# Performance work log

Hardware: AMD Instinct MI355X
Metric: run time of the kernel (lower is better)

## Reference

```python
import jax, jax.numpy as jnp
import numpy as np

MARGIN = 0.3
N_CLASSES = 256
N_SAMPLES = 32
D = 2048

def setup_inputs() -> dict:
    key = jax.random.key(0)
    k1, k2 = jax.random.split(key)
    embeddings = jax.random.normal(k1, (2 * N_CLASSES * N_SAMPLES, D), dtype=jnp.float32)
    target = jax.random.randint(k2, (2 * N_CLASSES * N_SAMPLES,), 0, N_CLASSES, dtype=jnp.int64 if jax.config.jax_enable_x64 else jnp.int32)
    return {"embeddings": embeddings, "target": target, "margin": MARGIN, "n_classes": N_CLASSES, "n_samples": N_SAMPLES}

def reference(embeddings, target, margin, n_classes, n_samples):
    # target is unused by the original forward (kept for signature fidelity).
    d = embeddings.shape[-1]
    # [C, 2, S, D]: slot 0 = positives, slot 1 = negatives per class
    e = embeddings.reshape(n_classes, 2, n_samples, d)
    pos, neg = e[:, 0], e[:, 1]                      # [C, S, D]
    anchor = pos.mean(axis=1, keepdims=True)          # [C, 1, D]
    ap = jnp.sqrt(jnp.sum((pos - anchor) ** 2, axis=-1))           # [C, S]
    neg_d2 = jnp.sum((neg - anchor) ** 2, axis=-1)                 # [C, S]
    # hardest negative: min squared distance to anchor -> its sqrt is an_distance
    an = jnp.sqrt(jnp.min(neg_d2, axis=1, keepdims=True))          # [C, 1]
    losses = jnp.sum(jax.nn.relu(ap - an + margin) ** 2, axis=1)   # [C]
    return losses.mean()
```

## Files before the change

kernel.cpp:

```cpp
#include <hip/hip_runtime.h>

#define NCLS 256
#define NSMP 32
#define DIM  2048
#define DV   (DIM / 4)
#define BLK  512
#define ROWS 520
#define PF   8

__global__ __launch_bounds__(BLK, 2)
void ccl_kernel(const float* __restrict__ emb,
                const float* __restrict__ margin_p,
                float* __restrict__ out) {
    const int c   = blockIdx.x;
    const int tid = threadIdx.x;

    __shared__ float part[NSMP * ROWS];
    __shared__ float d2p[NSMP];
    __shared__ float d2n[NSMP];

    const float4* pos = (const float4*)(emb + (size_t)c * 2 * NSMP * DIM);
    const float4* neg = pos + (size_t)NSMP * DV;

    float4 x[NSMP];
    #pragma unroll
    for (int i = 0; i < NSMP; ++i) x[i] = pos[(size_t)i * DV + tid];

    float4 a = make_float4(0.f, 0.f, 0.f, 0.f);
    #pragma unroll
    for (int i = 0; i < NSMP; ++i) {
        a.x += x[i].x; a.y += x[i].y; a.z += x[i].z; a.w += x[i].w;
    }
    const float inv = 1.0f / (float)NSMP;
    a.x *= inv; a.y *= inv; a.z *= inv; a.w *= inv;

    float4 nb[PF];
    #pragma unroll
    for (int j = 0; j < PF; ++j) nb[j] = neg[(size_t)j * DV + tid];

    #pragma unroll
    for (int i = 0; i < NSMP; ++i) {
        float dx = x[i].x - a.x, dy = x[i].y - a.y;
        float dz = x[i].z - a.z, dw = x[i].w - a.w;
        part[i * ROWS + tid] = dx * dx + dy * dy + dz * dz + dw * dw;
    }
    __syncthreads();

    const int s   = tid >> 4;
    const int c16 = tid & 15;
    {
        float sum = 0.f;
        #pragma unroll
        for (int k = 0; k < 8; ++k) {
            float4 v = *(const float4*)&part[s * ROWS + c16 * 4 + k * 64];
            sum += v.x + v.y + v.z + v.w;
        }
        #pragma unroll
        for (int off = 8; off >= 1; off >>= 1) sum += __shfl_xor(sum, off, 64);
        if (c16 == 0) d2p[s] = sum;
    }
    __syncthreads();

    #pragma unroll
    for (int i = 0; i < NSMP; ++i) {
        float4 n = nb[i & (PF - 1)];
        if (i + PF < NSMP) nb[i & (PF - 1)] = neg[(size_t)(i + PF) * DV + tid];
        float dx = n.x - a.x, dy = n.y - a.y;
        float dz = n.z - a.z, dw = n.w - a.w;
        part[i * ROWS + tid] = dx * dx + dy * dy + dz * dz + dw * dw;
    }
    __syncthreads();

    {
        float sum = 0.f;
        #pragma unroll
        for (int k = 0; k < 8; ++k) {
            float4 v = *(const float4*)&part[s * ROWS + c16 * 4 + k * 64];
            sum += v.x + v.y + v.z + v.w;
        }
        #pragma unroll
        for (int off = 8; off >= 1; off >>= 1) sum += __shfl_xor(sum, off, 64);
        if (c16 == 0) d2n[s] = sum;
    }
    __syncthreads();

    if (tid < 64) {
        float nd = (tid < NSMP) ? d2n[tid] : 3.4e38f;
        #pragma unroll
        for (int off = 32; off >= 1; off >>= 1) nd = fminf(nd, __shfl_xor(nd, off, 64));
        const float an = sqrtf(nd);
        const float margin = margin_p[0];

        float l = 0.f;
        if (tid < NSMP) {
            float ap = sqrtf(d2p[tid]);
            float v  = fmaxf(ap - an + margin, 0.f);
            l = v * v;
        }
        #pragma unroll
        for (int off = 32; off >= 1; off >>= 1) l += __shfl_xor(l, off, 64);
        if (tid == 0) atomicAdd(out, l * (1.0f / (float)NCLS));
    }
}

extern "C" void kernel_launch(void* const* d_in, const int* in_sizes, int n_in,
                              void* d_out, int out_size, void* d_ws, size_t ws_size,
                              hipStream_t stream) {
    const float* emb    = (const float*)d_in[0];
    const float* margin = (const float*)d_in[2];
    float* out = (float*)d_out;

    hipMemsetAsync(out, 0, sizeof(float), stream);
    ccl_kernel<<<NCLS, BLK, 0, stream>>>(emb, margin, out);
}
```

Measured before the change: 198.0 us.

## Split feature dimension across two blocks per class with a separate finalize kernel

Each class is now handled by two 256-thread blocks, each covering half of the feature dimension. Per-sample partial squared distances are combined with atomics into a workspace buffer. A second single-block kernel then computes the hardest negative, the hinge loss and the mean. This halves per-block shared memory and gives finer scheduling granularity, but adds a workspace memset, atomics and an extra kernel launch.

```diff
diff --git a/kernel.cpp b/kernel.cpp
--- a/kernel.cpp
+++ b/kernel.cpp
@@ -1,26 +1,28 @@
 #include <hip/hip_runtime.h>
 
-#define NCLS 256
-#define NSMP 32
-#define DIM  2048
-#define DV   (DIM / 4)
-#define BLK  512
-#define ROWS 520
-#define PF   8
+#define NCLS  256
+#define NSMP  32
+#define DIM   2048
+#define DV    (DIM / 4)
+#define SPLIT 2
+#define CHUNK (DV / SPLIT)
+#define BLK   256
+#define ROWS  264
+#define PF    8
 
 __global__ __launch_bounds__(BLK, 2)
-void ccl_kernel(const float* __restrict__ emb,
-                const float* __restrict__ margin_p,
-                float* __restrict__ out) {
+void ccl_partial(const float* __restrict__ emb,
+                 float* __restrict__ ws_pos,
+                 float* __restrict__ ws_neg) {
     const int c   = blockIdx.x;
+    const int h   = blockIdx.y;
     const int tid = threadIdx.x;
 
     __shared__ float part[NSMP * ROWS];
-    __shared__ float d2p[NSMP];
-    __shared__ float d2n[NSMP];
 
-    const float4* pos = (const float4*)(emb + (size_t)c * 2 * NSMP * DIM);
-    const float4* neg = pos + (size_t)NSMP * DV;
+    const float* base = emb + (size_t)c * 2 * NSMP * DIM + (size_t)h * (CHUNK * 4);
+    const float4* pos = (const float4*)base;
+    const float4* neg = (const float4*)(base + (size_t)NSMP * DIM);
 
     float4 x[NSMP];
     #pragma unroll
@@ -46,18 +48,18 @@
     }
     __syncthreads();
 
-    const int s   = tid >> 4;
-    const int c16 = tid & 15;
+    const int s  = tid >> 3;
+    const int c8 = tid & 7;
     {
         float sum = 0.f;
         #pragma unroll
         for (int k = 0; k < 8; ++k) {
-            float4 v = *(const float4*)&part[s * ROWS + c16 * 4 + k * 64];
+            float4 v = *(const float4*)&part[s * ROWS + c8 * 4 + k * 32];
             sum += v.x + v.y + v.z + v.w;
         }
         #pragma unroll
-        for (int off = 8; off >= 1; off >>= 1) sum += __shfl_xor(sum, off, 64);
-        if (c16 == 0) d2p[s] = sum;
+        for (int off = 4; off >= 1; off >>= 1) sum += __shfl_xor(sum, off, 64);
+        if (c8 == 0) atomicAdd(&ws_pos[c * NSMP + s], sum);
     }
     __syncthreads();
 
@@ -75,31 +77,49 @@
         float sum = 0.f;
         #pragma unroll
         for (int k = 0; k < 8; ++k) {
-            float4 v = *(const float4*)&part[s * ROWS + c16 * 4 + k * 64];
+            float4 v = *(const float4*)&part[s * ROWS + c8 * 4 + k * 32];
             sum += v.x + v.y + v.z + v.w;
         }
         #pragma unroll
-        for (int off = 8; off >= 1; off >>= 1) sum += __shfl_xor(sum, off, 64);
-        if (c16 == 0) d2n[s] = sum;
+        for (int off = 4; off >= 1; off >>= 1) sum += __shfl_xor(sum, off, 64);
+        if (c8 == 0) atomicAdd(&ws_neg[c * NSMP + s], sum);
     }
+}
+
+__global__ __launch_bounds__(NCLS)
+void ccl_final(const float* __restrict__ ws_pos,
+               const float* __restrict__ ws_neg,
+               const float* __restrict__ margin_p,
+               float* __restrict__ out) {
+    const int c    = threadIdx.x;
+    const int wave = c >> 6;
+    const int lane = c & 63;
+    __shared__ float red[NCLS / 64];
+
+    const float margin = margin_p[0];
+
+    float nd = 3.4e38f;
+    #pragma unroll
+    for (int i = 0; i < NSMP; ++i) nd = fminf(nd, ws_neg[c * NSMP + i]);
+    const float an = sqrtf(nd);
+
+    float l = 0.f;
+    #pragma unroll
+    for (int i = 0; i < NSMP; ++i) {
+        float ap = sqrtf(ws_pos[c * NSMP + i]);
+        float v  = fmaxf(ap - an + margin, 0.f);
+        l += v * v;
+    }
+
+    #pragma unroll
+    for (int off = 32; off >= 1; off >>= 1) l += __shfl_xor(l, off, 64);
+    if (lane == 0) red[wave] = l;
     __syncthreads();
-
-    if (tid < 64) {
-        float nd = (tid < NSMP) ? d2n[tid] : 3.4e38f;
+    if (c == 0) {
+        float t = 0.f;
         #pragma unroll
-        for (int off = 32; off >= 1; off >>= 1) nd = fminf(nd, __shfl_xor(nd, off, 64));
-        const float an = sqrtf(nd);
-        const float margin = margin_p[0];
-
-        float l = 0.f;
-        if (tid < NSMP) {
-            float ap = sqrtf(d2p[tid]);
-            float v  = fmaxf(ap - an + margin, 0.f);
-            l = v * v;
-        }
-        #pragma unroll
-        for (int off = 32; off >= 1; off >>= 1) l += __shfl_xor(l, off, 64);
-        if (tid == 0) atomicAdd(out, l * (1.0f / (float)NCLS));
+        for (int w = 0; w < NCLS / 64; ++w) t += red[w];
+        out[0] = t * (1.0f / (float)NCLS);
     }
 }
 
@@ -110,6 +130,12 @@
     const float* margin = (const float*)d_in[2];
     float* out = (float*)d_out;
 
-    hipMemsetAsync(out, 0, sizeof(float), stream);
-    ccl_kernel<<<NCLS, BLK, 0, stream>>>(emb, margin, out);
+    float* ws_pos = (float*)d_ws;
+    float* ws_neg = ws_pos + NCLS * NSMP;
+
+    hipMemsetAsync(d_ws, 0, 2 * NCLS * NSMP * sizeof(float), stream);
+
+    dim3 grid(NCLS, SPLIT);
+    ccl_partial<<<grid, BLK, 0, stream>>>(emb, ws_pos, ws_neg);
+    ccl_final<<<1, NCLS, 0, stream>>>(ws_pos, ws_neg, margin, out);
 }
```

After: 200.7 us. Within noise of the previous version (+1.4%).
